# Kernel optimization log

Hardware: AMD Instinct MI355X
Metric: run time of the kernel (lower is better)

## Reference

```python
import jax, jax.numpy as jnp
import numpy as np

HID = 50
IN_DIM = 20
OUT_DIM = 8


def lstm_cell(x, h, c, Wih, Whh, bih, bhh):
    # PyTorch LSTMCell: gates ordered i, f, g, o
    gates = x @ Wih.T + bih + h @ Whh.T + bhh  # [B, 4*HID]
    i, f, g, o = jnp.split(gates, 4, axis=-1)
    i = jax.nn.sigmoid(i)
    f = jax.nn.sigmoid(f)
    g = jnp.tanh(g)
    o = jax.nn.sigmoid(o)
    c_new = f * c + i * g
    h_new = o * jnp.tanh(c_new)
    return h_new, c_new


def setup_inputs() -> dict:
    key = jax.random.key(0)
    ks = jax.random.split(key, 16)
    s = 1.0 / np.sqrt(HID)
    u = lambda k, shape, bound: jax.random.uniform(k, shape, jnp.float32, -bound, bound)
    inp = {
        "x": jax.random.normal(ks[0], (512, 1024, IN_DIM), jnp.float32),
        "W1": u(ks[1], (HID, IN_DIM), 1.0 / np.sqrt(IN_DIM)),
        "b1": u(ks[2], (HID,), 1.0 / np.sqrt(IN_DIM)),
        "Wih1": u(ks[3], (4 * HID, HID), s), "Whh1": u(ks[4], (4 * HID, HID), s),
        "bih1": u(ks[5], (4 * HID,), s), "bhh1": u(ks[6], (4 * HID,), s),
        "Wih2": u(ks[7], (4 * HID, HID), s), "Whh2": u(ks[8], (4 * HID, HID), s),
        "bih2": u(ks[9], (4 * HID,), s), "bhh2": u(ks[10], (4 * HID,), s),
        "Wih3": u(ks[11], (4 * HID, HID), s), "Whh3": u(ks[12], (4 * HID, HID), s),
        "bih3": u(ks[13], (4 * HID,), s), "bhh3": u(ks[14], (4 * HID,), s),
        "W2": u(ks[15], (OUT_DIM, HID), s),
        "b2": jnp.zeros((OUT_DIM,), jnp.float32),
    }
    return inp


def reference(x, W1, b1, Wih1, Whh1, bih1, bhh1, Wih2, Whh2, bih2, bhh2,
              Wih3, Whh3, bih3, bhh3, W2, b2):
    B, T, _ = x.shape
    # Precompute the input projection for all timesteps (linear1)
    hid_all = x @ W1.T + b1  # [B, T, HID]
    z = jnp.zeros((B, HID), x.dtype)
    # carry replicates the original's (buggy) state handling:
    #   h3, c2 = lstm3(h2, (h3, c3)); c3 is never updated (stays zero)
    def step(carry, hid_t):
        h1, c1, h2, c2, h3, c3 = carry
        h1, c1 = lstm_cell(hid_t, h1, c1, Wih1, Whh1, bih1, bhh1)
        h2, c2 = lstm_cell(h1, h2, c2, Wih2, Whh2, bih2, bhh2)
        h3, c2 = lstm_cell(h2, h3, c3, Wih3, Whh3, bih3, bhh3)
        out = h3 @ W2.T + b2
        return (h1, c1, h2, c2, h3, c3), out

    _, outs = jax.lax.scan(step, (z, z, z, z, z, z),
                           jnp.swapaxes(hid_all, 0, 1))  # scan over time
    return jnp.swapaxes(outs, 0, 1)  # [B, T, OUT_DIM]
```

## Files before the change

kernel.cpp:

```cpp
#include <hip/hip_runtime.h>


#define T_SEQ 1024
#define IN_DIM 20
#define OUT_DIM 8

#define XC   0
#define CS   96
#define XH2  192
#define XH3  322
#define SMSZ 450

typedef float f32x2 __attribute__((ext_vector_type(2)));
typedef float f32x4 __attribute__((ext_vector_type(4)));

__device__ __forceinline__ void pkfma_lo(f32x2& d, f32x2 w, f32x2 u) {
    asm("v_pk_fma_f32 %0, %1, %2, %0 op_sel:[0,0,0] op_sel_hi:[0,1,1]"
        : "+v"(d) : "v"(w), "v"(u));
}
__device__ __forceinline__ void pkfma_hi(f32x2& d, f32x2 w, f32x2 u) {
    asm("v_pk_fma_f32 %0, %1, %2, %0 op_sel:[1,0,0] op_sel_hi:[1,1,1]"
        : "+v"(d) : "v"(w), "v"(u));
}
__device__ __forceinline__ void pkfma(f32x2& d, f32x2 a, f32x2 b) {
    asm("v_pk_fma_f32 %0, %1, %2, %0" : "+v"(d) : "v"(a), "v"(b));
}
__device__ __forceinline__ float sigm(float x) {
    return __builtin_amdgcn_rcpf(1.0f + __expf(-x));
}
__device__ __forceinline__ float tanh_f(float x) {
    return fmaf(2.0f, sigm(2.0f * x), -1.0f);
}
__device__ __forceinline__ f32x2 sigm2(f32x2 v, float b) {
    f32x2 r; r.x = sigm(v.x + b); r.y = sigm(v.y + b); return r;
}
__device__ __forceinline__ f32x2 tanh2(f32x2 v, float b) {
    f32x2 r; r.x = tanh_f(v.x + b); r.y = tanh_f(v.y + b); return r;
}
template <int CTRL>
__device__ __forceinline__ f32x2 dpp2(f32x2 v) {
    f32x2 r;
    r.x = __int_as_float(__builtin_amdgcn_mov_dpp(__float_as_int(v.x), CTRL, 0xF, 0xF, true));
    r.y = __int_as_float(__builtin_amdgcn_mov_dpp(__float_as_int(v.y), CTRL, 0xF, 0xF, true));
    return r;
}
__device__ __forceinline__ f32x2 swzx4(f32x2 v) {
    f32x2 r;
    r.x = __int_as_float(__builtin_amdgcn_ds_swizzle(__float_as_int(v.x), 0x101F));
    r.y = __int_as_float(__builtin_amdgcn_ds_swizzle(__float_as_int(v.y), 0x101F));
    return r;
}

__global__ __launch_bounds__(512, 2)
__attribute__((amdgpu_waves_per_eu(2, 2)))
void lstm_net_kernel(
    const float* __restrict__ x,
    const float* __restrict__ W1,   const float* __restrict__ b1,
    const float* __restrict__ Wih1, const float* __restrict__ Whh1,
    const float* __restrict__ bih1, const float* __restrict__ bhh1,
    const float* __restrict__ Wih2, const float* __restrict__ Whh2,
    const float* __restrict__ bih2, const float* __restrict__ bhh2,
    const float* __restrict__ Wih3, const float* __restrict__ Whh3,
    const float* __restrict__ bih3, const float* __restrict__ bhh3,
    const float* __restrict__ W2,   const float* __restrict__ b2,
    float* __restrict__ out)
{
    __shared__ __align__(16) f32x2 sm2[SMSZ];

    const int tid = threadIdx.x;
    const int b0  = blockIdx.x * 2;

    for (int i = tid; i < SMSZ; i += 512) sm2[i] = (f32x2){0.f, 0.f};
    __syncthreads();

    f32x2 wv[72];
    #pragma unroll
    for (int i = 0; i < 72; i++) wv[i] = (f32x2){0.f, 0.f};
    float bias4[4] = {0.f, 0.f, 0.f, 0.f};
    int   sel = 0, boff = 0, u = 0, loc = 0, ok = 0, sd = 0;
    bool  isOct = false, isL3 = false;
    f32x2 c1 = {0.f, 0.f};
    f32x2 xs[5];
    #pragma unroll
    for (int i = 0; i < 5; i++) xs[i] = (f32x2){0.f, 0.f};

    if (tid < 400) {
        isOct = true;
        u = tid >> 3; loc = tid & 7; isL3 = (loc >= 4);
        const int r = loc & 3, side = r >> 1, chunk = r & 1;
        const float* src = isL3 ? (side ? Whh3 : Wih3) : (side ? Whh2 : Wih2);
        const float* bi  = isL3 ? bih3 : bih2;
        const float* bh  = isL3 ? bhh3 : bhh2;
        const int row4[4] = {u, 50 + u, 100 + u, 150 + u};
        #pragma unroll
        for (int m = 0; m < 4; m++) {
            const bool dead = isL3 && (m == 1);
            const int row = row4[m];
            #pragma unroll
            for (int i = 0; i < 18; i++) {
                const int k0 = 2 * i, k1 = 2 * i + 1;
                const int d0 = 26 * chunk + k0, d1 = 26 * chunk + k1;
                const float w0 = (!dead && k0 < 26 && d0 < 50) ? src[row * 50 + d0] : 0.f;
                const float w1 = (!dead && k1 < 26 && d1 < 50) ? src[row * 50 + d1] : 0.f;
                wv[m * 18 + i] = (f32x2){w0, w1};
            }
            bias4[m] = dead ? 0.f : bi[row] + bh[row];
        }
        if (!isL3) { sel = side ? 1 : 0; boff = side ? 26 * chunk : 20 + 26 * chunk; }
        else       { sel = side ? 2 : 1; boff = 26 * chunk; }
    } else if (tid < 500) {
        u = (tid - 400) >> 1;
        const int h = tid & 1;
        sel = 0; boff = 36 * h;
        const int row4[4] = {u, 50 + u, 100 + u, 150 + u};
        #pragma unroll
        for (int m = 0; m < 4; m++) {
            const int row = row4[m];
            float bs = bih1[row] + bhh1[row];
            for (int j = 0; j < 50; j++) bs = fmaf(Wih1[row * 50 + j], b1[j], bs);
            bias4[m] = bs;
            if (h == 0) {
                float a20[20];
                #pragma unroll
                for (int k = 0; k < 20; k++) a20[k] = 0.f;
                for (int j = 0; j < 50; j++) {
                    const float a = Wih1[row * 50 + j];
                    const float* w1r = W1 + j * 20;
                    #pragma unroll
                    for (int k = 0; k < 20; k++) a20[k] = fmaf(a, w1r[k], a20[k]);
                }
                #pragma unroll
                for (int i = 0; i < 18; i++) {
                    const int k0 = 2 * i, k1 = 2 * i + 1;
                    const float w0 = (k0 < 20) ? a20[k0] : Whh1[row * 50 + (k0 - 20)];
                    const float w1 = (k1 < 20) ? a20[k1] : Whh1[row * 50 + (k1 - 20)];
                    wv[m * 18 + i] = (f32x2){w0, w1};
                }
            } else {
                #pragma unroll
                for (int i = 0; i < 18; i++) {
                    const int k0 = 2 * i, k1 = 2 * i + 1;
                    const float w0 = (k0 < 34) ? Whh1[row * 50 + 16 + k0] : 0.f;
                    const float w1 = (k1 < 34) ? Whh1[row * 50 + 16 + k1] : 0.f;
                    wv[m * 18 + i] = (f32x2){w0, w1};
                }
            }
        }
    } else if (tid < 508) {
        ok = tid - 500;
        #pragma unroll
        for (int i = 0; i < 26; i++) {
            const int d0 = 2 * i, d1 = 2 * i + 1;
            const float w0 = (d0 < 50) ? W2[ok * 50 + d0] : 0.f;
            const float w1 = (d1 < 50) ? W2[ok * 50 + d1] : 0.f;
            wv[i] = (f32x2){w0, w1};
        }
        bias4[0] = b2[ok];
    } else {
        sd = tid - 508;
        for (int t = 0; t < 3; t++) {
            #pragma unroll
            for (int i = 0; i < 5; i++) {
                const int dim = sd + 4 * i;
                f32x2 v;
                v.x = x[((size_t)b0 * T_SEQ + t) * IN_DIM + dim];
                v.y = x[((size_t)(b0 + 1) * T_SEQ + t) * IN_DIM + dim];
                if (t < 2) sm2[XC + t * CS + dim] = v;
                else       xs[i] = v;
            }
        }
    }
    __syncthreads();

    for (int s = 0; s < T_SEQ + 3; ++s) {
        const int p = s & 1, pm = p ^ 1;

        if (tid < 500) {
            const int base = ((sel == 0) ? (XC + p * CS)
                            : (sel == 1) ? (XH2 + p * 64)
                                         : (XH3 + pm * 64)) + boff;
            const f32x4* B4 = (const f32x4*)(sm2 + base);
            f32x2 A0 = {0.f,0.f}, A1 = {0.f,0.f}, A2 = {0.f,0.f}, A3 = {0.f,0.f};
            #pragma unroll
            for (int i = 0; i < 18; i++) {
                const f32x4 uu = B4[i];
                const f32x2 ul = uu.lo, uh = uu.hi;
                pkfma_lo(A0, wv[i],      ul); pkfma_hi(A0, wv[i],      uh);
                pkfma_lo(A1, wv[18 + i], ul); pkfma_hi(A1, wv[18 + i], uh);
                pkfma_lo(A2, wv[36 + i], ul); pkfma_hi(A2, wv[36 + i], uh);
                pkfma_lo(A3, wv[54 + i], ul); pkfma_hi(A3, wv[54 + i], uh);
            }
            A0 += dpp2<0xB1>(A0); A1 += dpp2<0xB1>(A1);
            A2 += dpp2<0xB1>(A2); A3 += dpp2<0xB1>(A3);
            if (isOct) {
                A0 += dpp2<0x4E>(A0); A1 += dpp2<0x4E>(A1);
                A2 += dpp2<0x4E>(A2); A3 += dpp2<0x4E>(A3);
            }
            const f32x2 ii = sigm2(A0, bias4[0]);
            const f32x2 ff = sigm2(A1, bias4[1]);
            const f32x2 gg = tanh2(A2, bias4[2]);
            const f32x2 oo = sigm2(A3, bias4[3]);
            f32x2 P = ii * gg;

            if (isOct) {
                const bool valid3 = (s >= 2) && (s < T_SEQ + 2);
                f32x2 ps = P;
                if (isL3 && !valid3) ps = (f32x2){0.f, 0.f};
                const f32x2 t4 = swzx4(ps);
                if (loc == 0) {
                    if (s >= 1 && s <= T_SEQ) {
                        f32x2 c2 = P;
                        pkfma(c2, ff, t4);
                        f32x2 hh;
                        hh.x = oo.x * tanh_f(c2.x);
                        hh.y = oo.y * tanh_f(c2.y);
                        sm2[XH2 + pm * 64 + u] = hh;
                    }
                } else if (loc == 4) {
                    if (valid3) {
                        f32x2 hh;
                        hh.x = oo.x * tanh_f(P.x);
                        hh.y = oo.y * tanh_f(P.y);
                        sm2[XH3 + p * 64 + u] = hh;
                    }
                }
            } else {
                if ((tid & 1) == 0 && s < T_SEQ) {
                    f32x2 cn = P;
                    pkfma(cn, ff, c1);
                    c1 = cn;
                    f32x2 hh;
                    hh.x = oo.x * tanh_f(c1.x);
                    hh.y = oo.y * tanh_f(c1.y);
                    sm2[XC + pm * CS + 20 + u] = hh;
                }
            }
        } else if (tid < 508) {
            if (s >= 3) {
                const int t = s - 3;
                const f32x4* H4 = (const f32x4*)(sm2 + XH3 + pm * 64);
                f32x2 a0 = {0.f, 0.f}, a1 = {0.f, 0.f};
                #pragma unroll
                for (int i = 0; i < 26; i++) {
                    const f32x4 uu = H4[i];
                    pkfma_lo(a0, wv[i], uu.lo);
                    pkfma_hi(a1, wv[i], uu.hi);
                }
                const f32x2 acc = a0 + a1;
                out[((size_t)b0 * T_SEQ + t) * OUT_DIM + ok]       = acc.x + bias4[0];
                out[((size_t)(b0 + 1) * T_SEQ + t) * OUT_DIM + ok] = acc.y + bias4[0];
            }
        } else {
            if (s >= 1 && s + 1 < T_SEQ) {
                #pragma unroll
                for (int i = 0; i < 5; i++)
                    sm2[XC + pm * CS + sd + 4 * i] = xs[i];
            }
            if (s + 2 < T_SEQ) {
                const int t = s + 2;
                #pragma unroll
                for (int i = 0; i < 5; i++) {
                    const int dim = sd + 4 * i;
                    xs[i].x = x[((size_t)b0 * T_SEQ + t) * IN_DIM + dim];
                    xs[i].y = x[((size_t)(b0 + 1) * T_SEQ + t) * IN_DIM + dim];
                }
            }
        }
        __syncthreads();
    }
}

extern "C" void kernel_launch(void* const* d_in, const int* in_sizes, int n_in,
                              void* d_out, int out_size, void* d_ws, size_t ws_size,
                              hipStream_t stream) {
    const float* x    = (const float*)d_in[0];
    const float* W1   = (const float*)d_in[1];
    const float* b1   = (const float*)d_in[2];
    const float* Wih1 = (const float*)d_in[3];
    const float* Whh1 = (const float*)d_in[4];
    const float* bih1 = (const float*)d_in[5];
    const float* bhh1 = (const float*)d_in[6];
    const float* Wih2 = (const float*)d_in[7];
    const float* Whh2 = (const float*)d_in[8];
    const float* bih2 = (const float*)d_in[9];
    const float* bhh2 = (const float*)d_in[10];
    const float* Wih3 = (const float*)d_in[11];
    const float* Whh3 = (const float*)d_in[12];
    const float* bih3 = (const float*)d_in[13];
    const float* bhh3 = (const float*)d_in[14];
    const float* W2   = (const float*)d_in[15];
    const float* b2   = (const float*)d_in[16];
    float* out = (float*)d_out;

    dim3 grid(256), block(512);
    lstm_net_kernel<<<grid, block, 0, stream>>>(
        x, W1, b1, Wih1, Whh1, bih1, bhh1, Wih2, Whh2, bih2, bhh2,
        Wih3, Whh3, bih3, bhh3, W2, b2, out);
}
```

Baseline: 1.727 ms.

## Switch shared state to planar per-batch layout with float4 dot products

Result: slower. 1.764 ms (+2.1%).

```diff
diff --git a/kernel.cpp b/kernel.cpp
--- a/kernel.cpp
+++ b/kernel.cpp
@@ -5,26 +5,14 @@
 #define IN_DIM 20
 #define OUT_DIM 8
 
-#define XC   0
-#define CS   96
-#define XH2  192
-#define XH3  322
-#define SMSZ 450
+#define CF   0
+#define FH2  384
+#define FH3  648
+#define SMSZ 904
 
 typedef float f32x2 __attribute__((ext_vector_type(2)));
 typedef float f32x4 __attribute__((ext_vector_type(4)));
 
-__device__ __forceinline__ void pkfma_lo(f32x2& d, f32x2 w, f32x2 u) {
-    asm("v_pk_fma_f32 %0, %1, %2, %0 op_sel:[0,0,0] op_sel_hi:[0,1,1]"
-        : "+v"(d) : "v"(w), "v"(u));
-}
-__device__ __forceinline__ void pkfma_hi(f32x2& d, f32x2 w, f32x2 u) {
-    asm("v_pk_fma_f32 %0, %1, %2, %0 op_sel:[1,0,0] op_sel_hi:[1,1,1]"
-        : "+v"(d) : "v"(w), "v"(u));
-}
-__device__ __forceinline__ void pkfma(f32x2& d, f32x2 a, f32x2 b) {
-    asm("v_pk_fma_f32 %0, %1, %2, %0" : "+v"(d) : "v"(a), "v"(b));
-}
 __device__ __forceinline__ float sigm(float x) {
     return __builtin_amdgcn_rcpf(1.0f + __expf(-x));
 }
@@ -34,8 +22,9 @@
 __device__ __forceinline__ f32x2 sigm2(f32x2 v, float b) {
     f32x2 r; r.x = sigm(v.x + b); r.y = sigm(v.y + b); return r;
 }
-__device__ __forceinline__ f32x2 tanh2(f32x2 v, float b) {
-    f32x2 r; r.x = tanh_f(v.x + b); r.y = tanh_f(v.y + b); return r;
+__device__ __forceinline__ float hsum4(f32x4 v) {
+    const f32x2 t = v.lo + v.hi;
+    return t.x + t.y;
 }
 template <int CTRL>
 __device__ __forceinline__ f32x2 dpp2(f32x2 v) {
@@ -65,17 +54,17 @@
     const float* __restrict__ W2,   const float* __restrict__ b2,
     float* __restrict__ out)
 {
-    __shared__ __align__(16) f32x2 sm2[SMSZ];
+    __shared__ __align__(16) float smf[SMSZ];
 
     const int tid = threadIdx.x;
     const int b0  = blockIdx.x * 2;
 
-    for (int i = tid; i < SMSZ; i += 512) sm2[i] = (f32x2){0.f, 0.f};
+    for (int i = tid; i < SMSZ; i += 512) smf[i] = 0.f;
     __syncthreads();
 
-    f32x2 wv[72];
+    f32x4 wv4[36];
     #pragma unroll
-    for (int i = 0; i < 72; i++) wv[i] = (f32x2){0.f, 0.f};
+    for (int i = 0; i < 36; i++) wv4[i] = (f32x4){0.f, 0.f, 0.f, 0.f};
     float bias4[4] = {0.f, 0.f, 0.f, 0.f};
     int   sel = 0, boff = 0, u = 0, loc = 0, ok = 0, sd = 0;
     bool  isOct = false, isL3 = false;
@@ -88,6 +77,7 @@
         isOct = true;
         u = tid >> 3; loc = tid & 7; isL3 = (loc >= 4);
         const int r = loc & 3, side = r >> 1, chunk = r & 1;
+        const int cb = 28 * chunk;
         const float* src = isL3 ? (side ? Whh3 : Wih3) : (side ? Whh2 : Wih2);
         const float* bi  = isL3 ? bih3 : bih2;
         const float* bh  = isL3 ? bhh3 : bhh2;
@@ -97,17 +87,20 @@
             const bool dead = isL3 && (m == 1);
             const int row = row4[m];
             #pragma unroll
-            for (int i = 0; i < 18; i++) {
-                const int k0 = 2 * i, k1 = 2 * i + 1;
-                const int d0 = 26 * chunk + k0, d1 = 26 * chunk + k1;
-                const float w0 = (!dead && k0 < 26 && d0 < 50) ? src[row * 50 + d0] : 0.f;
-                const float w1 = (!dead && k1 < 26 && d1 < 50) ? src[row * 50 + d1] : 0.f;
-                wv[m * 18 + i] = (f32x2){w0, w1};
+            for (int i = 0; i < 9; i++) {
+                f32x4 w = {0.f, 0.f, 0.f, 0.f};
+                #pragma unroll
+                for (int e = 0; e < 4; e++) {
+                    const int k = 4 * i + e;
+                    const int d = cb + k;
+                    if (!dead && k < 28 && d < 50) w[e] = src[row * 50 + d];
+                }
+                wv4[m * 9 + i] = w;
             }
             bias4[m] = dead ? 0.f : bi[row] + bh[row];
         }
-        if (!isL3) { sel = side ? 1 : 0; boff = side ? 26 * chunk : 20 + 26 * chunk; }
-        else       { sel = side ? 2 : 1; boff = 26 * chunk; }
+        if (!isL3) { sel = side ? 1 : 0; boff = side ? cb : 20 + cb; }
+        else       { sel = side ? 2 : 1; boff = cb; }
     } else if (tid < 500) {
         u = (tid - 400) >> 1;
         const int h = tid & 1;
@@ -130,30 +123,39 @@
                     for (int k = 0; k < 20; k++) a20[k] = fmaf(a, w1r[k], a20[k]);
                 }
                 #pragma unroll
-                for (int i = 0; i < 18; i++) {
-                    const int k0 = 2 * i, k1 = 2 * i + 1;
-                    const float w0 = (k0 < 20) ? a20[k0] : Whh1[row * 50 + (k0 - 20)];
-                    const float w1 = (k1 < 20) ? a20[k1] : Whh1[row * 50 + (k1 - 20)];
-                    wv[m * 18 + i] = (f32x2){w0, w1};
+                for (int i = 0; i < 9; i++) {
+                    f32x4 w;
+                    #pragma unroll
+                    for (int e = 0; e < 4; e++) {
+                        const int d = 4 * i + e;
+                        w[e] = (d < 20) ? a20[d] : Whh1[row * 50 + (d - 20)];
+                    }
+                    wv4[m * 9 + i] = w;
                 }
             } else {
                 #pragma unroll
-                for (int i = 0; i < 18; i++) {
-                    const int k0 = 2 * i, k1 = 2 * i + 1;
-                    const float w0 = (k0 < 34) ? Whh1[row * 50 + 16 + k0] : 0.f;
-                    const float w1 = (k1 < 34) ? Whh1[row * 50 + 16 + k1] : 0.f;
-                    wv[m * 18 + i] = (f32x2){w0, w1};
+                for (int i = 0; i < 9; i++) {
+                    f32x4 w = {0.f, 0.f, 0.f, 0.f};
+                    #pragma unroll
+                    for (int e = 0; e < 4; e++) {
+                        const int d = 36 + 4 * i + e;
+                        if (d < 70) w[e] = Whh1[row * 50 + (d - 20)];
+                    }
+                    wv4[m * 9 + i] = w;
                 }
             }
         }
     } else if (tid < 508) {
         ok = tid - 500;
         #pragma unroll
-        for (int i = 0; i < 26; i++) {
-            const int d0 = 2 * i, d1 = 2 * i + 1;
-            const float w0 = (d0 < 50) ? W2[ok * 50 + d0] : 0.f;
-            const float w1 = (d1 < 50) ? W2[ok * 50 + d1] : 0.f;
-            wv[i] = (f32x2){w0, w1};
+        for (int i = 0; i < 13; i++) {
+            f32x4 w = {0.f, 0.f, 0.f, 0.f};
+            #pragma unroll
+            for (int e = 0; e < 4; e++) {
+                const int d = 4 * i + e;
+                if (d < 50) w[e] = W2[ok * 50 + d];
+            }
+            wv4[i] = w;
         }
         bias4[0] = b2[ok];
     } else {
@@ -165,8 +167,10 @@
                 f32x2 v;
                 v.x = x[((size_t)b0 * T_SEQ + t) * IN_DIM + dim];
                 v.y = x[((size_t)(b0 + 1) * T_SEQ + t) * IN_DIM + dim];
-                if (t < 2) sm2[XC + t * CS + dim] = v;
-                else       xs[i] = v;
+                if (t < 2) {
+                    smf[CF + t * 192 + dim]      = v.x;
+                    smf[CF + t * 192 + 96 + dim] = v.y;
+                } else xs[i] = v;
             }
         }
     }
@@ -176,20 +180,30 @@
         const int p = s & 1, pm = p ^ 1;
 
         if (tid < 500) {
-            const int base = ((sel == 0) ? (XC + p * CS)
-                            : (sel == 1) ? (XH2 + p * 64)
-                                         : (XH3 + pm * 64)) + boff;
-            const f32x4* B4 = (const f32x4*)(sm2 + base);
-            f32x2 A0 = {0.f,0.f}, A1 = {0.f,0.f}, A2 = {0.f,0.f}, A3 = {0.f,0.f};
+            const int bstr = (sel == 0) ? 96 : 64;
+            const float* bp = smf
+                + ((sel == 0) ? (CF + p * 192)
+                 : (sel == 1) ? (FH2 + p * 128)
+                              : (FH3 + pm * 128)) + boff;
+            const f32x4* B0 = (const f32x4*)bp;
+            const f32x4* B1 = (const f32x4*)(bp + bstr);
+            f32x4 q00 = {0,0,0,0}, q01 = {0,0,0,0};
+            f32x4 q10 = {0,0,0,0}, q11 = {0,0,0,0};
+            f32x4 q20 = {0,0,0,0}, q21 = {0,0,0,0};
+            f32x4 q30 = {0,0,0,0}, q31 = {0,0,0,0};
             #pragma unroll
-            for (int i = 0; i < 18; i++) {
-                const f32x4 uu = B4[i];
-                const f32x2 ul = uu.lo, uh = uu.hi;
-                pkfma_lo(A0, wv[i],      ul); pkfma_hi(A0, wv[i],      uh);
-                pkfma_lo(A1, wv[18 + i], ul); pkfma_hi(A1, wv[18 + i], uh);
-                pkfma_lo(A2, wv[36 + i], ul); pkfma_hi(A2, wv[36 + i], uh);
-                pkfma_lo(A3, wv[54 + i], ul); pkfma_hi(A3, wv[54 + i], uh);
-            }
+            for (int i = 0; i < 9; i++) {
+                const f32x4 u0 = B0[i], u1 = B1[i];
+                q00 += wv4[i]      * u0;  q01 += wv4[i]      * u1;
+                q10 += wv4[9 + i]  * u0;  q11 += wv4[9 + i]  * u1;
+                q20 += wv4[18 + i] * u0;  q21 += wv4[18 + i] * u1;
+                q30 += wv4[27 + i] * u0;  q31 += wv4[27 + i] * u1;
+            }
+            f32x2 A0 = {hsum4(q00), hsum4(q01)};
+            f32x2 A1 = {hsum4(q10), hsum4(q11)};
+            f32x2 A2 = {hsum4(q20), hsum4(q21)};
+            f32x2 A3 = {hsum4(q30), hsum4(q31)};
+
             A0 += dpp2<0xB1>(A0); A1 += dpp2<0xB1>(A1);
             A2 += dpp2<0xB1>(A2); A3 += dpp2<0xB1>(A3);
             if (isOct) {
@@ -198,7 +212,9 @@
             }
             const f32x2 ii = sigm2(A0, bias4[0]);
             const f32x2 ff = sigm2(A1, bias4[1]);
-            const f32x2 gg = tanh2(A2, bias4[2]);
+            f32x2 gg;
+            gg.x = tanh_f(A2.x + bias4[2]);
+            gg.y = tanh_f(A2.y + bias4[2]);
             const f32x2 oo = sigm2(A3, bias4[3]);
             f32x2 P = ii * gg;
 
@@ -209,52 +225,50 @@
                 const f32x2 t4 = swzx4(ps);
                 if (loc == 0) {
                     if (s >= 1 && s <= T_SEQ) {
-                        f32x2 c2 = P;
-                        pkfma(c2, ff, t4);
-                        f32x2 hh;
-                        hh.x = oo.x * tanh_f(c2.x);
-                        hh.y = oo.y * tanh_f(c2.y);
-                        sm2[XH2 + pm * 64 + u] = hh;
+                        f32x2 c2;
+                        c2.x = fmaf(ff.x, t4.x, P.x);
+                        c2.y = fmaf(ff.y, t4.y, P.y);
+                        smf[FH2 + pm * 128 + u]      = oo.x * tanh_f(c2.x);
+                        smf[FH2 + pm * 128 + 64 + u] = oo.y * tanh_f(c2.y);
                     }
                 } else if (loc == 4) {
                     if (valid3) {
-                        f32x2 hh;
-                        hh.x = oo.x * tanh_f(P.x);
-                        hh.y = oo.y * tanh_f(P.y);
-                        sm2[XH3 + p * 64 + u] = hh;
+                        smf[FH3 + p * 128 + u]      = oo.x * tanh_f(P.x);
+                        smf[FH3 + p * 128 + 64 + u] = oo.y * tanh_f(P.y);
                     }
                 }
             } else {
                 if ((tid & 1) == 0 && s < T_SEQ) {
-                    f32x2 cn = P;
-                    pkfma(cn, ff, c1);
+                    f32x2 cn;
+                    cn.x = fmaf(ff.x, c1.x, P.x);
+                    cn.y = fmaf(ff.y, c1.y, P.y);
                     c1 = cn;
-                    f32x2 hh;
-                    hh.x = oo.x * tanh_f(c1.x);
-                    hh.y = oo.y * tanh_f(c1.y);
-                    sm2[XC + pm * CS + 20 + u] = hh;
+                    smf[CF + pm * 192 + 20 + u]      = oo.x * tanh_f(c1.x);
+                    smf[CF + pm * 192 + 96 + 20 + u] = oo.y * tanh_f(c1.y);
                 }
             }
         } else if (tid < 508) {
             if (s >= 3) {
                 const int t = s - 3;
-                const f32x4* H4 = (const f32x4*)(sm2 + XH3 + pm * 64);
-                f32x2 a0 = {0.f, 0.f}, a1 = {0.f, 0.f};
-                #pragma unroll
-                for (int i = 0; i < 26; i++) {
-                    const f32x4 uu = H4[i];
-                    pkfma_lo(a0, wv[i], uu.lo);
-                    pkfma_hi(a1, wv[i], uu.hi);
-                }
-                const f32x2 acc = a0 + a1;
-                out[((size_t)b0 * T_SEQ + t) * OUT_DIM + ok]       = acc.x + bias4[0];
-                out[((size_t)(b0 + 1) * T_SEQ + t) * OUT_DIM + ok] = acc.y + bias4[0];
+                const f32x4* H0 = (const f32x4*)(smf + FH3 + pm * 128);
+                const f32x4* H1 = (const f32x4*)(smf + FH3 + pm * 128 + 64);
+                f32x4 a0 = {0,0,0,0}, a1 = {0,0,0,0};
+                #pragma unroll
+                for (int i = 0; i < 13; i++) {
+                    a0 += wv4[i] * H0[i];
+                    a1 += wv4[i] * H1[i];
+                }
+                out[((size_t)b0 * T_SEQ + t) * OUT_DIM + ok]       = hsum4(a0) + bias4[0];
+                out[((size_t)(b0 + 1) * T_SEQ + t) * OUT_DIM + ok] = hsum4(a1) + bias4[0];
             }
         } else {
             if (s >= 1 && s + 1 < T_SEQ) {
                 #pragma unroll
-                for (int i = 0; i < 5; i++)
-                    sm2[XC + pm * CS + sd + 4 * i] = xs[i];
+                for (int i = 0; i < 5; i++) {
+                    const int dim = sd + 4 * i;
+                    smf[CF + pm * 192 + dim]      = xs[i].x;
+                    smf[CF + pm * 192 + 96 + dim] = xs[i].y;
+                }
             }
             if (s + 2 < T_SEQ) {
                 const int t = s + 2;
```
